# Optimization experiments

Measured on AMD Instinct MI355X. Metric: run time of the kernel, lower is better.

The kernel has to match this reference:

```python
import jax, jax.numpy as jnp
import numpy as np

IN_CH = 512
OUT_CH = 512
NUM_GROUPS = 32
EPS = 1e-5


def setup_inputs() -> dict:
    key = jax.random.key(0)
    ks = jax.random.split(key, 8)
    N, C, H, W = 4, IN_CH, 64, 64
    s = 0.02
    return {
        "x": jax.random.normal(ks[0], (N, C, H, W), jnp.float32),
        "gn_scale": jnp.ones((C,), jnp.float32),
        "gn_bias": jnp.zeros((C,), jnp.float32),
        "wq": jax.random.normal(ks[1], (OUT_CH, C), jnp.float32) * s,
        "bq": jnp.zeros((OUT_CH,), jnp.float32),
        "wk": jax.random.normal(ks[2], (OUT_CH, C), jnp.float32) * s,
        "bk": jnp.zeros((OUT_CH,), jnp.float32),
        "wv": jax.random.normal(ks[3], (OUT_CH, C), jnp.float32) * s,
        "bv": jnp.zeros((OUT_CH,), jnp.float32),
        "wo": jax.random.normal(ks[4], (OUT_CH, OUT_CH), jnp.float32) * s,
        "bo": jnp.zeros((OUT_CH,), jnp.float32),
    }


def _group_norm(x, scale, bias):
    # x: [N, C, H, W] -> normalize per (group, spatial)
    N, C, H, W = x.shape
    g = x.reshape(N, NUM_GROUPS, C // NUM_GROUPS, H, W)
    mean = jnp.mean(g, axis=(2, 3, 4), keepdims=True)
    var = jnp.var(g, axis=(2, 3, 4), keepdims=True)
    g = (g - mean) * jax.lax.rsqrt(var + EPS)
    h = g.reshape(N, C, H, W)
    return h * scale[None, :, None, None] + bias[None, :, None, None]


def _conv1x1(x, w, b):
    # x: [N, C_in, H, W], w: [C_out, C_in] -> [N, C_out, H, W]
    return jnp.einsum('nchw,dc->ndhw', x, w) + b[None, :, None, None]


def reference(x, gn_scale, gn_bias, wq, bq, wk, bk, wv, bv, wo, bo):
    N, C, H, W = x.shape
    L = H * W
    h = _group_norm(x, gn_scale, gn_bias)
    q = _conv1x1(h, wq, bq).reshape(N, OUT_CH, L)
    k = _conv1x1(h, wk, bk).reshape(N, OUT_CH, L)
    v = _conv1x1(h, wv, bv).reshape(N, OUT_CH, L)
    scores = jnp.einsum('nci,ncj->nij', q, k) * (OUT_CH ** -0.5)  # [N, L, L]
    att = jax.nn.softmax(scores, axis=-1)
    out = jnp.einsum('nij,ncj->nci', att, v).reshape(N, OUT_CH, H, W)
    out = _conv1x1(out, wo, bo)
    return out + x  # skip_proj is Identity since in_ch == out_ch
```

## Files before the change

### kernel.cpp

```cpp
#include <hip/hip_runtime.h>
#include <math.h>

#define NB   4
#define CCH  512
#define LL   4096
#define GRP  32
#define CPG  16
#define CL   (CCH*LL)
#define EPSV 1e-5f
#define QSTR 1024

typedef __bf16 bf16x8 __attribute__((ext_vector_type(8)));
typedef float  f32x4  __attribute__((ext_vector_type(4)));

#define GLOAD_LDS16(g, l) __builtin_amdgcn_global_load_lds( \
    (const __attribute__((address_space(1))) void*)(g),     \
    (__attribute__((address_space(3))) void*)(l), 16, 0, 0)

__device__ __forceinline__ int swz_slot(int row, int q) {
    return 4 * row + (q ^ ((row >> 1) & 3));
}
__device__ __forceinline__ void swz_src(int l, int& jj, int& cc) {
    jj = l >> 2;
    cc = (l & 3) ^ ((l >> 3) & 3);
}

#define DPPF(x, ctrl) __builtin_bit_cast(float, \
    __builtin_amdgcn_update_dpp(0, __builtin_bit_cast(int, (x)), (ctrl), 0xf, 0xf, false))
__device__ __forceinline__ float red_sum16(float x) {
    x += DPPF(x, 0xB1); x += DPPF(x, 0x4E);
    x += DPPF(x, 0x124); x += DPPF(x, 0x128);
    return x;
}

__global__ __launch_bounds__(1024) void gn_stats(const float* __restrict__ x,
                                                 float* __restrict__ stats) {
    int gid = blockIdx.x >> 1, h = blockIdx.x & 1;
    int n = gid >> 5, g = gid & 31;
    size_t base = ((size_t)n * CCH + (size_t)g * CPG) * LL
                + (size_t)h * (CPG * LL / 2);
    const float4* xp = (const float4*)(x + base);
    const int NV = CPG * LL / 8;
    int tid = threadIdx.x;
    float s1 = 0.f, s2 = 0.f;
    for (int i = tid; i < NV; i += 1024) {
        float4 v = xp[i];
        s1 += v.x + v.y + v.z + v.w;
        s2 += v.x*v.x + v.y*v.y + v.z*v.z + v.w*v.w;
    }
    __shared__ float red[32];
    for (int o = 32; o; o >>= 1) { s1 += __shfl_down(s1, o); s2 += __shfl_down(s2, o); }
    int lane = tid & 63, w = tid >> 6;
    if (!lane) { red[w] = s1; red[16 + w] = s2; }
    __syncthreads();
    if (tid == 0) {
        float a = 0.f, b = 0.f;
        for (int i = 0; i < 16; ++i) { a += red[i]; b += red[16 + i]; }
        stats[gid * 4 + h * 2]     = a;
        stats[gid * 4 + h * 2 + 1] = b;
    }
}

__global__ __launch_bounds__(256) void gn_norm_t(const float* __restrict__ x,
    const float* __restrict__ gamma, const float* __restrict__ beta,
    const float* __restrict__ stats, __bf16* __restrict__ Ht) {
    __shared__ float T[64][65];
    int n = blockIdx.z, c0 = blockIdx.y * 64, l0 = blockIdx.x * 64;
    int tid = threadIdx.x;
    int lx = tid & 63, py = tid >> 6;
    const float* xb = x + (size_t)n * CL;
    const float inv_n = 1.f / (float)(CPG * LL);
#pragma unroll
    for (int p = 0; p < 16; ++p) {
        int cl = p * 4 + py;
        int c = c0 + cl;
        int g = c >> 4;
        const float* P = stats + (size_t)(n * GRP + g) * 4;
        float s1 = P[0] + P[2], s2 = P[1] + P[3];
        float mean = s1 * inv_n;
        float var  = s2 * inv_n - mean * mean;
        float rstd = rsqrtf(var + EPSV);
        float sc = gamma[c] * rstd, bi = beta[c] - mean * sc;
        float v = xb[(size_t)c * LL + l0 + lx];
        T[lx][cl] = v * sc + bi;
    }
    __syncthreads();
    __bf16* hb = Ht + (size_t)n * CL;
    const int sub  = tid & 7;
    const int lrow = tid >> 3;
#pragma unroll
    for (int p = 0; p < 2; ++p) {
        int ll = p * 32 + lrow;
        bf16x8 v;
#pragma unroll
        for (int s = 0; s < 8; ++s) v[s] = (__bf16)T[ll][sub * 8 + s];
        *(bf16x8*)(hb + (size_t)(l0 + ll) * CCH + c0 + sub * 8) = v;
    }
}

__global__ __launch_bounds__(256) void tobf16_4(
    const float* __restrict__ s0, const float* __restrict__ s1,
    const float* __restrict__ s2, const float* __restrict__ s3,
    __bf16* __restrict__ dst) {
    const float* sp = (blockIdx.y == 0) ? s0 : (blockIdx.y == 1) ? s1
                    : (blockIdx.y == 2) ? s2 : s3;
    int i = (blockIdx.x * 256 + threadIdx.x) * 4;
    float4 v = *(const float4*)(sp + i);
    __bf16* d = dst + (size_t)blockIdx.y * CCH * CCH + i;
    d[0] = (__bf16)v.x; d[1] = (__bf16)v.y; d[2] = (__bf16)v.z; d[3] = (__bf16)v.w;
}

#define BM 128
#define BN 128
#define BK 64

template<int EPI>
__device__ __forceinline__ void gemm_body(
    __bf16* As, __bf16* Bs,
    const __bf16* __restrict__ A, const __bf16* __restrict__ B,
    void* __restrict__ Cv, int M, int N, int K,
    long bsA, long bsB, long bsC, long bsR,
    const float* __restrict__ bias, const float* __restrict__ bias2,
    const float* __restrict__ resid,
    int bx, int by, int bz)
{
    const int tid = threadIdx.x;
    const int l = tid & 63, w = tid >> 6;
    const int wm = w >> 1, wn = w & 1;
    const int m0 = by * BM, n0 = bx * BN;
    A += (long)bz * bsA;
    B += (long)bz * bsB;

    f32x4 acc[4][4];
#pragma unroll
    for (int i = 0; i < 4; ++i)
#pragma unroll
        for (int j = 0; j < 4; ++j) acc[i][j] = f32x4{0.f, 0.f, 0.f, 0.f};

    int jj, cc; swz_src(l, jj, cc);
    const int slot = swz_slot(l & 15, l >> 4);

    const __bf16* Ag = A + (size_t)(m0 + w * 16 + jj) * K + cc * 8;
    const __bf16* Bg = B + (size_t)(n0 + w * 16 + jj) * K + cc * 8;
    char* AsB = (char*)As + w * 1024;
    char* BsB = (char*)Bs + w * 1024;

    for (int k0 = 0; k0 < K; k0 += BK) {
        GLOAD_LDS16(Ag + k0,                      AsB);
        GLOAD_LDS16(Ag + k0 + (size_t)64*K,       AsB + 4096);
        GLOAD_LDS16(Bg + k0,                      BsB);
        GLOAD_LDS16(Bg + k0 + (size_t)64*K,       BsB + 4096);
        GLOAD_LDS16(Ag + k0 + 32,                 AsB + 8192);
        GLOAD_LDS16(Ag + k0 + 32 + (size_t)64*K,  AsB + 8192 + 4096);
        GLOAD_LDS16(Bg + k0 + 32,                 BsB + 8192);
        GLOAD_LDS16(Bg + k0 + 32 + (size_t)64*K,  BsB + 8192 + 4096);
        __syncthreads();
#pragma unroll
        for (int h = 0; h < 2; ++h) {
            bf16x8 ar[4], br[4];
#pragma unroll
            for (int t = 0; t < 4; ++t) {
                ar[t] = *(const bf16x8*)(As + h*4096 + (wm*64 + t*16) * 32 + slot * 8);
                br[t] = *(const bf16x8*)(Bs + h*4096 + (wn*64 + t*16) * 32 + slot * 8);
            }
#pragma unroll
            for (int ti = 0; ti < 4; ++ti)
#pragma unroll
                for (int tj = 0; tj < 4; ++tj)
                    acc[ti][tj] = __builtin_amdgcn_mfma_f32_16x16x32_bf16(
                        ar[ti], br[tj], acc[ti][tj], 0, 0, 0);
        }
        __syncthreads();
    }

    const long cb = (long)bz * bsC;
    const float* bn = (EPI == 5) ? ((n0 < 512) ? bias : (bias2 - 512)) : nullptr;
#pragma unroll
    for (int ti = 0; ti < 4; ++ti) {
#pragma unroll
        for (int r = 0; r < 4; ++r) {
            int m = m0 + wm*64 + ti*16 + (l >> 4)*4 + r;
            float bv = (EPI == 2 || EPI == 4) ? bias[m] : 0.f;
#pragma unroll
            for (int tj = 0; tj < 4; ++tj) {
                int n = n0 + wn*64 + tj*16 + (l & 15);
                float v = acc[ti][tj][r];
                if (EPI == 5) v += bn[n];
                if (EPI == 2 || EPI == 4) v += bv;
                if (EPI == 4) {
                    float rs = resid[(long)bz * bsR + (size_t)m * N + n];
                    ((float*)Cv)[cb + (size_t)m * N + n] = v + rs;
                } else {
                    ((__bf16*)Cv)[cb + (size_t)m * N + n] = (__bf16)v;
                }
            }
        }
    }
}

__global__ __launch_bounds__(256) void gemm_qkv(
    const __bf16* __restrict__ Ht, const __bf16* __restrict__ wqkb,
    __bf16* __restrict__ QKt, const __bf16* __restrict__ wvb,
    __bf16* __restrict__ Vb,
    const float* __restrict__ bq, const float* __restrict__ bk,
    const float* __restrict__ bv)
{
    __shared__ __align__(16) __bf16 As[2 * BM * 32];
    __shared__ __align__(16) __bf16 Bs[2 * BN * 32];
    const int d = blockIdx.x;
    const int wk = (d & 7) * 192 + (d >> 3);
    if (wk < 1024) {
        gemm_body<5>(As, Bs, Ht, wqkb, QKt, LL, 1024, CCH,
                     CL, 0, (long)LL * 1024, 0, bq, bk, nullptr,
                     wk & 7, (wk >> 3) & 31, wk >> 8);
    } else {
        const int v = wk - 1024;
        gemm_body<2>(As, Bs, wvb, Ht, Vb, CCH, LL, CCH,
                     0, CL, CL, 0, bv, nullptr, nullptr,
                     v & 31, (v >> 5) & 3, v >> 7);
    }
}

__global__ __launch_bounds__(256) void gemm_out(
    const __bf16* __restrict__ wob, const __bf16* __restrict__ Ot,
    float* __restrict__ out, const float* __restrict__ bo,
    const float* __restrict__ xr)
{
    __shared__ __align__(16) __bf16 As[2 * BM * 32];
    __shared__ __align__(16) __bf16 Bs[2 * BN * 32];
    const int d = blockIdx.x;
    const int wk = (d & 7) * 64 + (d >> 3);
    gemm_body<4>(As, Bs, wob, Ot, (void*)out, CCH, LL, CCH,
                 0, CL, CL, CL, bo, nullptr, xr,
                 wk & 31, (wk >> 5) & 3, wk >> 7);
}

#define PSTR 88

__global__ __launch_bounds__(512, 2) void flash_attn(
    const __bf16* __restrict__ QK, const __bf16* __restrict__ Vb,
    __bf16* __restrict__ Ot)
{
    __shared__ __align__(16) __bf16 Ks[16 * 64 * 32];
    __shared__ __align__(16) __bf16 Vs[2 * 512 * 32];
    __shared__ float  Sm[64 * 68];
    __shared__ __align__(16) __bf16 Ps[64 * PSTR];
    __shared__ float Lp[64 * 2];

    const int tid = threadIdx.x;
    const int l = tid & 63, w = tid >> 6;
    const int wi = w & 1, jh = (w >> 1) & 1, kh = w >> 2;
    const int g = l >> 4, c = l & 15;
    const int b = (blockIdx.x & 7) >> 1;
    const int qt = ((blockIdx.x >> 3) << 1) | (blockIdx.x & 1);
    const int i0 = qt * 64;
    const size_t bb2 = (size_t)b * LL * QSTR;
    const size_t bb  = (size_t)b * CL;
    const float alpha = 0.044194173824159216f;

    int jj, cc; swz_src(l, jj, cc);
    const int slot = swz_slot(c, g);

    bf16x8 Qf[2][8];
    {
        const __bf16* Qg = QK + bb2 + (size_t)(i0 + wi*32 + c) * QSTR + kh*256 + g*8;
#pragma unroll
        for (int mi = 0; mi < 2; ++mi)
#pragma unroll
            for (int kc = 0; kc < 8; ++kc)
                Qf[mi][kc] = *(const bf16x8*)(Qg + (size_t)mi*16*QSTR + kc*32);
    }

    f32x4 Oacc[4][4];
#pragma unroll
    for (int mi = 0; mi < 4; ++mi)
#pragma unroll
        for (int ni = 0; ni < 4; ++ni) Oacc[mi][ni] = f32x4{0.f, 0.f, 0.f, 0.f};
    float l_r[4] = {0.f, 0.f, 0.f, 0.f};

    const __bf16* Kb = QK + bb2 + 512;
    const __bf16* Vg = Vb + bb;

    auto stageK = [&](int j0) {
#pragma unroll
        for (int q = 0; q < 2; ++q) {
            int kc = q * 8 + w;
#pragma unroll
            for (int p = 0; p < 4; ++p) {
                const __bf16* src = Kb + (size_t)(j0 + p*16 + jj) * QSTR + kc*32 + cc*8;
                GLOAD_LDS16(src, (char*)Ks + kc*4096 + p*1024);
            }
        }
    };
    auto stageV = [&](int j0) {
#pragma unroll
        for (int jc = 0; jc < 2; ++jc)
#pragma unroll
            for (int p = 0; p < 4; ++p) {
                const __bf16* src = Vg + (size_t)(w*64 + p*16 + jj) * LL + j0 + jc*32 + cc*8;
                GLOAD_LDS16(src, (char*)Vs + jc*32768 + (w*64 + p*16)*64);
            }
    };

    auto expst = [&](const f32x4 (&Sx)[2]) {
        const int er0 = wi*32 + (1 - kh)*16 + g*4;
#pragma unroll
        for (int tj = 0; tj < 2; ++tj)
#pragma unroll
            for (int r = 0; r < 4; ++r)
                Sm[(er0 + r)*68 + (jh*2 + tj)*16 + c] = Sx[tj][r];
    };
    auto smx = [&](const f32x4 (&Sown)[2]) {
        const int row0 = wi*32 + kh*16 + g*4;
#pragma unroll
        for (int r = 0; r < 4; ++r) {
            float rs = 0.f;
#pragma unroll
            for (int tj = 0; tj < 2; ++tj) {
                float p = __expf((Sown[tj][r] + Sm[(row0 + r)*68 + (jh*2 + tj)*16 + c]) * alpha);
                rs += p;
                Ps[(row0 + r) * PSTR + (jh*2 + tj)*16 + c] = (__bf16)p;
            }
            l_r[r] += rs;
        }
    };

    stageK(0);
    for (int t = 0; t < 64; ++t) {
        __syncthreads();
        stageV(t * 64);

        f32x4 S[2][2];
#pragma unroll
        for (int mi = 0; mi < 2; ++mi)
#pragma unroll
            for (int tj = 0; tj < 2; ++tj) S[mi][tj] = f32x4{0.f,0.f,0.f,0.f};
        __builtin_amdgcn_s_setprio(1);
#pragma unroll
        for (int kc = 0; kc < 8; ++kc) {
#pragma unroll
            for (int tj = 0; tj < 2; ++tj) {
                bf16x8 kf = *(const bf16x8*)(Ks + (kh*8 + kc)*2048 + (jh*2 + tj)*512 + slot*8);
#pragma unroll
                for (int mi = 0; mi < 2; ++mi)
                    S[mi][tj] = __builtin_amdgcn_mfma_f32_16x16x32_bf16(Qf[mi][kc], kf, S[mi][tj], 0, 0, 0);
            }
        }
        __builtin_amdgcn_s_setprio(0);

        if (kh) expst(S[0]); else expst(S[1]);
        __syncthreads();

        if (kh) smx(S[1]); else smx(S[0]);
        __syncthreads();
        if (t < 63) stageK((t + 1) * 64);

        __builtin_amdgcn_s_setprio(1);
#pragma unroll
        for (int jc = 0; jc < 2; ++jc) {
            bf16x8 pa[4];
#pragma unroll
            for (int mi = 0; mi < 4; ++mi)
                pa[mi] = *(const bf16x8*)(Ps + (mi*16 + c) * PSTR + jc*32 + g*8);
#pragma unroll
            for (int ni = 0; ni < 4; ++ni) {
                bf16x8 vf = *(const bf16x8*)(Vs + jc*16384 + (w*64 + ni*16)*32 + slot*8);
#pragma unroll
                for (int mi = 0; mi < 4; ++mi)
                    Oacc[mi][ni] = __builtin_amdgcn_mfma_f32_16x16x32_bf16(pa[mi], vf, Oacc[mi][ni], 0, 0, 0);
            }
        }
        __builtin_amdgcn_s_setprio(0);
    }

#pragma unroll
    for (int r = 0; r < 4; ++r) {
        float tot = red_sum16(l_r[r]);
        if (c == 0) Lp[(wi*32 + kh*16 + g*4 + r)*2 + jh] = tot;
    }
    __syncthreads();
#pragma unroll
    for (int mi = 0; mi < 4; ++mi) {
#pragma unroll
        for (int r = 0; r < 4; ++r) {
            int row = mi*16 + g*4 + r;
            float inv = 1.f / (Lp[row*2] + Lp[row*2 + 1]);
#pragma unroll
            for (int ni = 0; ni < 4; ++ni) {
                int col = w*64 + ni*16 + c;
                Ot[bb + (size_t)(i0 + row) * CCH + col] = (__bf16)(Oacc[mi][ni][r] * inv);
            }
        }
    }
}

extern "C" void kernel_launch(void* const* d_in, const int* in_sizes, int n_in,
                              void* d_out, int out_size, void* d_ws, size_t ws_size,
                              hipStream_t stream) {
    const float* x   = (const float*)d_in[0];
    const float* gnw = (const float*)d_in[1];
    const float* gnb = (const float*)d_in[2];
    const float* wq  = (const float*)d_in[3];
    const float* bq  = (const float*)d_in[4];
    const float* wk  = (const float*)d_in[5];
    const float* bk  = (const float*)d_in[6];
    const float* wv  = (const float*)d_in[7];
    const float* bv  = (const float*)d_in[8];
    const float* wo  = (const float*)d_in[9];
    const float* bo  = (const float*)d_in[10];
    float* out = (float*)d_out;

    __bf16* wsb = (__bf16*)d_ws;
    const size_t NCL = (size_t)NB * CL;
    __bf16* Ht  = wsb;
    __bf16* QKt = Ht + NCL;
    __bf16* Vb  = QKt + 2 * NCL;
    __bf16* Ot  = Vb + NCL;
    __bf16* Wb  = Ot + NCL;
    float* stats = (float*)(Wb + (size_t)4 * CCH * CCH);
    __bf16* wqkb = Wb;
    __bf16* wvb  = Wb + (size_t)2 * CCH * CCH;
    __bf16* wob  = Wb + (size_t)3 * CCH * CCH;

    tobf16_4<<<dim3(256, 4), 256, 0, stream>>>(wq, wk, wv, wo, Wb);
    gn_stats<<<NB * GRP * 2, 1024, 0, stream>>>(x, stats);
    gn_norm_t<<<dim3(LL / 64, CCH / 64, NB), 256, 0, stream>>>(x, gnw, gnb, stats, Ht);

    gemm_qkv<<<dim3(1536), 256, 0, stream>>>(Ht, wqkb, QKt, wvb, Vb, bq, bk, bv);

    flash_attn<<<dim3(256), 512, 0, stream>>>(QKt, Vb, Ot);

    gemm_out<<<dim3(512), 256, 0, stream>>>(wob, Ot, out, bo, x);
}
```

Baseline: 350.0 us.

## Fuse weight bf16 conversion into gn_stats and make QKV GEMM blocks do two tiles

Folds the four weight fp32-to-bf16 conversions into the group-norm stats kernel as four extra 1024-thread blocks, removing one kernel launch. The QKV GEMM now launches half as many blocks, and each block loops over two adjacent output tiles. This is meant to cut launch and tail overhead, but it lowers the number of blocks available for parallelism, and each conversion block now streams a whole weight matrix by itself.

```diff
diff --git a/kernel.cpp b/kernel.cpp
--- a/kernel.cpp
+++ b/kernel.cpp
@@ -11,6 +11,7 @@
 #define QSTR 1024
 
 typedef __bf16 bf16x8 __attribute__((ext_vector_type(8)));
+typedef __bf16 bf16x4 __attribute__((ext_vector_type(4)));
 typedef float  f32x4  __attribute__((ext_vector_type(4)));
 
 #define GLOAD_LDS16(g, l) __builtin_amdgcn_global_load_lds( \
@@ -33,8 +34,23 @@
     return x;
 }
 
-__global__ __launch_bounds__(1024) void gn_stats(const float* __restrict__ x,
-                                                 float* __restrict__ stats) {
+__global__ __launch_bounds__(1024) void gn_stats_w(const float* __restrict__ x,
+    float* __restrict__ stats,
+    const float* __restrict__ wq, const float* __restrict__ wk,
+    const float* __restrict__ wv, const float* __restrict__ wo,
+    __bf16* __restrict__ Wb) {
+    if (blockIdx.x >= 256) {
+        const int wi2 = blockIdx.x - 256;
+        const float* sp = (wi2 == 0) ? wq : (wi2 == 1) ? wk
+                        : (wi2 == 2) ? wv : wo;
+        __bf16* d = Wb + (size_t)wi2 * CCH * CCH;
+        for (int i = threadIdx.x * 4; i < CCH * CCH; i += 4096) {
+            float4 v = *(const float4*)(sp + i);
+            bf16x4 o; o[0]=(__bf16)v.x; o[1]=(__bf16)v.y; o[2]=(__bf16)v.z; o[3]=(__bf16)v.w;
+            *(bf16x4*)(d + i) = o;
+        }
+        return;
+    }
     int gid = blockIdx.x >> 1, h = blockIdx.x & 1;
     int n = gid >> 5, g = gid & 31;
     size_t base = ((size_t)n * CCH + (size_t)g * CPG) * LL
@@ -96,18 +112,6 @@
         for (int s = 0; s < 8; ++s) v[s] = (__bf16)T[ll][sub * 8 + s];
         *(bf16x8*)(hb + (size_t)(l0 + ll) * CCH + c0 + sub * 8) = v;
     }
-}
-
-__global__ __launch_bounds__(256) void tobf16_4(
-    const float* __restrict__ s0, const float* __restrict__ s1,
-    const float* __restrict__ s2, const float* __restrict__ s3,
-    __bf16* __restrict__ dst) {
-    const float* sp = (blockIdx.y == 0) ? s0 : (blockIdx.y == 1) ? s1
-                    : (blockIdx.y == 2) ? s2 : s3;
-    int i = (blockIdx.x * 256 + threadIdx.x) * 4;
-    float4 v = *(const float4*)(sp + i);
-    __bf16* d = dst + (size_t)blockIdx.y * CCH * CCH + i;
-    d[0] = (__bf16)v.x; d[1] = (__bf16)v.y; d[2] = (__bf16)v.z; d[3] = (__bf16)v.w;
 }
 
 #define BM 128
@@ -208,16 +212,20 @@
     __shared__ __align__(16) __bf16 As[2 * BM * 32];
     __shared__ __align__(16) __bf16 Bs[2 * BN * 32];
     const int d = blockIdx.x;
-    const int wk = (d & 7) * 192 + (d >> 3);
-    if (wk < 1024) {
-        gemm_body<5>(As, Bs, Ht, wqkb, QKt, LL, 1024, CCH,
-                     CL, 0, (long)LL * 1024, 0, bq, bk, nullptr,
-                     wk & 7, (wk >> 3) & 31, wk >> 8);
-    } else {
-        const int v = wk - 1024;
-        gemm_body<2>(As, Bs, wvb, Ht, Vb, CCH, LL, CCH,
-                     0, CL, CL, 0, bv, nullptr, nullptr,
-                     v & 31, (v >> 5) & 3, v >> 7);
+    const int base = (d & 7) * 192 + (d >> 3) * 2;
+#pragma unroll 1
+    for (int it = 0; it < 2; ++it) {
+        const int wk = base + it;
+        if (wk < 1024) {
+            gemm_body<5>(As, Bs, Ht, wqkb, QKt, LL, 1024, CCH,
+                         CL, 0, (long)LL * 1024, 0, bq, bk, nullptr,
+                         wk & 7, (wk >> 3) & 31, wk >> 8);
+        } else {
+            const int v = wk - 1024;
+            gemm_body<2>(As, Bs, wvb, Ht, Vb, CCH, LL, CCH,
+                         0, CL, CL, 0, bv, nullptr, nullptr,
+                         v & 31, (v >> 5) & 3, v >> 7);
+        }
     }
 }
 
@@ -422,11 +430,10 @@
     __bf16* wvb  = Wb + (size_t)2 * CCH * CCH;
     __bf16* wob  = Wb + (size_t)3 * CCH * CCH;
 
-    tobf16_4<<<dim3(256, 4), 256, 0, stream>>>(wq, wk, wv, wo, Wb);
-    gn_stats<<<NB * GRP * 2, 1024, 0, stream>>>(x, stats);
+    gn_stats_w<<<dim3(260), 1024, 0, stream>>>(x, stats, wq, wk, wv, wo, Wb);
     gn_norm_t<<<dim3(LL / 64, CCH / 64, NB), 256, 0, stream>>>(x, gnw, gnb, stats, Ht);
 
-    gemm_qkv<<<dim3(1536), 256, 0, stream>>>(Ht, wqkb, QKt, wvb, Vb, bq, bk, bv);
+    gemm_qkv<<<dim3(768), 256, 0, stream>>>(Ht, wqkb, QKt, wvb, Vb, bq, bk, bv);
 
     flash_attn<<<dim3(256), 512, 0, stream>>>(QKt, Vb, Ot);
 
```

New measurement: 385.3 us. +10.1%, slower.
